# Kernel tuning notes

Measured on AMD Instinct MI355X. Metric: run time of the kernel, lower is better.

## Reference

```python
import jax, jax.numpy as jnp
import numpy as np

B, T, P, C = 32, 16, 16, 2048
EPS = 1e-5


def setup_inputs() -> dict:
    key = jax.random.key(0)
    ks = jax.random.split(key, 9)
    s = 0.02
    return {
        "X": jax.random.normal(ks[0], (B, T, P, C), dtype=jnp.float32),
        "W_att": jax.random.normal(ks[1], (C, C), dtype=jnp.float32) * s,
        "b_att": jnp.zeros((C,), dtype=jnp.float32),
        "W1": jax.random.normal(ks[2], (C, C), dtype=jnp.float32) * s,
        "b1": jnp.zeros((C,), dtype=jnp.float32),
        "gamma": jnp.ones((C,), dtype=jnp.float32),
        "beta": jnp.zeros((C,), dtype=jnp.float32),
        "W2": jax.random.normal(ks[3], (C, C), dtype=jnp.float32) * s,
        "b2": jnp.zeros((C,), dtype=jnp.float32),
    }


def reference(X, W_att, b_att, W1, b1, gamma, beta, W2, b2):
    b, t, p, c = X.shape
    Xf = X.reshape(b * t, p, c)                                   # [BT, P, C]
    # per-frame attention gate: mean over parts -> Linear -> sigmoid
    attn = jax.nn.sigmoid(jnp.einsum("nc,dc->nd", Xf.mean(axis=1), W_att) + b_att)
    Xg = Xf * attn[:, None, :]                                    # gate each part
    # gcn: Linear -> per-frame BatchNorm1d (training stats over P) -> ReLU -> Linear
    h = jnp.einsum("npc,dc->npd", Xg, W1) + b1                    # [BT, P, C]
    mu = h.mean(axis=1, keepdims=True)
    var = jnp.mean(jnp.square(h - mu), axis=1, keepdims=True)     # biased var, as torch BN
    hn = (h - mu) * jax.lax.rsqrt(var + EPS) * gamma + beta
    out = jnp.einsum("npc,dc->npd", jax.nn.relu(hn), W2) + b2
    return out.reshape(b, t, p, c)
```

## Files before the change

kernel.cpp:

```cpp
#include <hip/hip_runtime.h>
#include <hip/hip_bf16.h>

typedef __attribute__((ext_vector_type(8))) short short8;
typedef __attribute__((ext_vector_type(4))) float f32x4;

static constexpr int Cdim = 2048;
static constexpr int NFRM = 512;
static constexpr int Pdim = 16;
static constexpr int MROWS = NFRM * Pdim;
static constexpr float EPS = 1e-5f;

__device__ __forceinline__ unsigned short f2b(float x) {
  union { float f; unsigned u; } v; v.f = x;
  unsigned r = v.u + 0x7fffu + ((v.u >> 16) & 1u);
  return (unsigned short)(r >> 16);
}

__device__ __forceinline__ void gload16(const void* g, void* l) {
  __builtin_amdgcn_global_load_lds(
      (const __attribute__((address_space(1))) unsigned int*)g,
      (__attribute__((address_space(3))) unsigned int*)l, 16, 0, 0);
}


__global__ __launch_bounds__(256) void cast3_kernel(
    const float* __restrict__ s0, const float* __restrict__ s1, const float* __restrict__ s2,
    unsigned short* __restrict__ d0, unsigned short* __restrict__ d1, unsigned short* __restrict__ d2)
{
  long i = (long)blockIdx.x * 256 + threadIdx.x;
  const float* s; unsigned short* d; long off;
  if (i < 1048576)      { s = s0; d = d0; off = i; }
  else if (i < 2097152) { s = s1; d = d1; off = i - 1048576; }
  else                  { s = s2; d = d2; off = i - 2097152; }
  float4 v = reinterpret_cast<const float4*>(s)[off];
  union { unsigned short u[4]; unsigned long long q; } o;
  o.u[0] = f2b(v.x); o.u[1] = f2b(v.y); o.u[2] = f2b(v.z); o.u[3] = f2b(v.w);
  *reinterpret_cast<unsigned long long*>(d + off * 4) = o.q;
}

__global__ __launch_bounds__(256) void mean_cast_kernel(
    const float* __restrict__ X, unsigned short* __restrict__ Mb)
{
  int idx = blockIdx.x * 256 + threadIdx.x;
  int n  = idx >> 9;
  int c4 = idx & 511;
  const float4* xp = reinterpret_cast<const float4*>(X) + (long)n * (Pdim * 512) + c4;
  float4 s = {0.f, 0.f, 0.f, 0.f};
  #pragma unroll
  for (int p = 0; p < Pdim; ++p) {
    float4 v = xp[(long)p * 512];
    s.x += v.x; s.y += v.y; s.z += v.z; s.w += v.w;
  }
  const float r = 1.f / 16.f;
  union { unsigned short u[4]; unsigned long long q; } o;
  o.u[0] = f2b(s.x * r); o.u[1] = f2b(s.y * r); o.u[2] = f2b(s.z * r); o.u[3] = f2b(s.w * r);
  *reinterpret_cast<unsigned long long*>(Mb + (long)idx * 4) = o.q;
}

__global__ __launch_bounds__(256) void gate_kernel(
    const float* __restrict__ X, const float* __restrict__ PA, const float* __restrict__ PB,
    const float* __restrict__ b_att, unsigned short* __restrict__ Xg)
{
  constexpr long F = 512L * 2048;
  long idx = (long)blockIdx.x * 256 + threadIdx.x;
  int c4 = (int)(idx & 511);
  long np = idx >> 9;
  long n  = np >> 4;
  float4 x  = reinterpret_cast<const float4*>(X)[idx];
  float4 p0 = reinterpret_cast<const float4*>(PA)[n * 512 + c4];
  float4 p1 = reinterpret_cast<const float4*>(PA + F)[n * 512 + c4];
  float4 p2 = reinterpret_cast<const float4*>(PB)[n * 512 + c4];
  float4 p3 = reinterpret_cast<const float4*>(PB + F)[n * 512 + c4];
  float4 bb = reinterpret_cast<const float4*>(b_att)[c4];
  float4 a;
  a.x = 1.f / (1.f + __expf(-(p0.x + p1.x + p2.x + p3.x + bb.x)));
  a.y = 1.f / (1.f + __expf(-(p0.y + p1.y + p2.y + p3.y + bb.y)));
  a.z = 1.f / (1.f + __expf(-(p0.z + p1.z + p2.z + p3.z + bb.z)));
  a.w = 1.f / (1.f + __expf(-(p0.w + p1.w + p2.w + p3.w + bb.w)));
  union { unsigned short u[4]; unsigned long long q; } o;
  o.u[0] = f2b(x.x * a.x); o.u[1] = f2b(x.y * a.y);
  o.u[2] = f2b(x.z * a.z); o.u[3] = f2b(x.w * a.w);
  *reinterpret_cast<unsigned long long*>(Xg + idx * 4) = o.q;
}

__global__ __launch_bounds__(256) void gemm_att_sk(
    const unsigned short* __restrict__ A,
    const unsigned short* __restrict__ B,
    float* __restrict__ PA, float* __restrict__ PB)
{
  constexpr int N = 2048, K = 2048, KH = 512;
  constexpr long F = 512L * 2048;
  __shared__ unsigned short As[128 * 32];
  __shared__ unsigned short Bs[128 * 32];
  const int t = threadIdx.x;
  const int lane = t & 63;
  const int wid = t >> 6;
  const int wr = wid >> 1, wc = wid & 1;
  const int m0 = blockIdx.x * 128, n0 = blockIdx.y * 128;
  const int k0 = blockIdx.z * KH;
  float* out = (blockIdx.z < 2) ? (PA + (long)blockIdx.z * F) : (PB + (long)(blockIdx.z - 2) * F);

  f32x4 acc[4][4];
  #pragma unroll
  for (int i = 0; i < 4; i++)
    #pragma unroll
    for (int j = 0; j < 4; j++) acc[i][j] = (f32x4){0.f, 0.f, 0.f, 0.f};

  const int srow = t >> 2;
  const int scol = (t & 3) * 8;
  const long aoff0 = (long)(m0 + srow) * K + scol;
  const long aoff1 = (long)(m0 + 64 + srow) * K + scol;
  const long boff0 = (long)(n0 + srow) * K + scol;
  const long boff1 = (long)(n0 + 64 + srow) * K + scol;
  char* AsB = (char*)As;
  char* BsB = (char*)Bs;

  const int fr = lane & 15;
  const int fk = (lane >> 4) * 8;

  for (int kt = k0; kt < k0 + KH; kt += 32) {
    __syncthreads();
    gload16(A + aoff0 + kt, AsB + t * 16);
    gload16(A + aoff1 + kt, AsB + 4096 + t * 16);
    gload16(B + boff0 + kt, BsB + t * 16);
    gload16(B + boff1 + kt, BsB + 4096 + t * 16);
    __syncthreads();
    short8 af[4], bfr[4];
    #pragma unroll
    for (int m = 0; m < 4; m++)
      af[m] = *reinterpret_cast<const short8*>(&As[(wr * 64 + m * 16 + fr) * 32 + fk]);
    #pragma unroll
    for (int n = 0; n < 4; n++)
      bfr[n] = *reinterpret_cast<const short8*>(&Bs[(wc * 64 + n * 16 + fr) * 32 + fk]);
    #pragma unroll
    for (int m = 0; m < 4; m++)
      #pragma unroll
      for (int n = 0; n < 4; n++)
        acc[m][n] = __builtin_amdgcn_mfma_f32_16x16x32_bf16(af[m], bfr[n], acc[m][n], 0, 0, 0);
  }

  const int l4 = lane >> 4;
  #pragma unroll
  for (int m = 0; m < 4; m++) {
    const int r0 = m0 + wr * 64 + m * 16 + l4 * 4;
    #pragma unroll
    for (int n = 0; n < 4; n++) {
      const int cn = n0 + wc * 64 + n * 16 + fr;
      #pragma unroll
      for (int j = 0; j < 4; j++)
        out[(long)(r0 + j) * N + cn] = acc[m][n][j];
    }
  }
}

template<int EPI>
__global__ __launch_bounds__(512, 2) void gemm256(
    const unsigned short* __restrict__ A,
    const unsigned short* __restrict__ Bp,
    int Kk, int Nn, int nbx,
    const float* __restrict__ bias,
    const float* __restrict__ gamma,
    const float* __restrict__ beta,
    float* __restrict__ Cf,
    unsigned short* __restrict__ Cb)
{
  __shared__ char lds[131072];
  const int t = threadIdx.x;
  const int lane = t & 63;
  const int wid = t >> 6;
  const int wr = wid >> 2;
  const int wc = wid & 3;

  const int nw = gridDim.x;
  const int wg = (blockIdx.x & 7) * (nw >> 3) + (blockIdx.x >> 3);
  const int bx = wg % nbx;
  const int by = wg / nbx;
  const int m0 = bx << 8, n0 = by << 8;

  const int NT = Kk >> 6;
  const int NI = NT >> 1;

  const long h64 = (long)64 * Kk, h128 = (long)128 * Kk;
  const int row0 = t >> 3;
  const int col0 = ((t & 7) * 8) ^ ((row0 & 7) << 3);
  const unsigned short* gA = A  + (long)(m0 + row0) * Kk + col0;
  const unsigned short* gB = Bp + (long)(n0 + row0) * Kk + col0;

  const int fr_ = lane & 15;
  const int cb0 = ((lane >> 4) << 4) ^ ((fr_ & 7) << 4);
  const int aB = (wr << 14) + fr_ * 128;
  const int bB = 32768 + ((wc >> 1) << 14) + ((wc & 1) << 13) + fr_ * 128;

#define STG(gp_, ko_, lo_) do { \
    const unsigned short* g0_ = (gp_) + (ko_); \
    gload16(g0_, lds + (lo_) + (t << 4)); \
    gload16(g0_ + h64, lds + (lo_) + 8192 + (t << 4)); } while (0)

#define LDSA(buf_, m_, ks_) (*(const short8*)(lds + (buf_) * 65536 + aB + (m_) * 2048 + (cb0 ^ ((ks_) << 6))))
#define LDSB(buf_, n_, ks_) (*(const short8*)(lds + (buf_) * 65536 + bB + (n_) * 2048 + (cb0 ^ ((ks_) << 6))))

#define RDAF(buf_, mb_) do { \
    af[0][0] = LDSA(buf_, (mb_) + 0, 0); af[0][1] = LDSA(buf_, (mb_) + 0, 1); \
    af[1][0] = LDSA(buf_, (mb_) + 1, 0); af[1][1] = LDSA(buf_, (mb_) + 1, 1); \
    af[2][0] = LDSA(buf_, (mb_) + 2, 0); af[2][1] = LDSA(buf_, (mb_) + 2, 1); \
    af[3][0] = LDSA(buf_, (mb_) + 3, 0); af[3][1] = LDSA(buf_, (mb_) + 3, 1); } while (0)

#define RDB(buf_, nb_, dst_) do { \
    dst_[0][0] = LDSB(buf_, (nb_) + 0, 0); dst_[0][1] = LDSB(buf_, (nb_) + 0, 1); \
    dst_[1][0] = LDSB(buf_, (nb_) + 1, 0); dst_[1][1] = LDSB(buf_, (nb_) + 1, 1); } while (0)

#define QUAD(mb_, nb_, b_) do { \
    _Pragma("unroll") \
    for (int mi = 0; mi < 4; ++mi) { \
      _Pragma("unroll") \
      for (int ni = 0; ni < 2; ++ni) { \
        acc[(mb_) + mi][(nb_) + ni] = __builtin_amdgcn_mfma_f32_16x16x32_bf16(af[mi][0], b_[ni][0], acc[(mb_) + mi][(nb_) + ni], 0, 0, 0); \
        acc[(mb_) + mi][(nb_) + ni] = __builtin_amdgcn_mfma_f32_16x16x32_bf16(af[mi][1], b_[ni][1], acc[(mb_) + mi][(nb_) + ni], 0, 0, 0); \
      } } } while (0)

#define BARX() do { \
    __builtin_amdgcn_sched_barrier(0); \
    __builtin_amdgcn_s_barrier(); \
    __builtin_amdgcn_sched_barrier(0); } while (0)

#define PRIO1() __builtin_amdgcn_s_setprio(1)
#define PRIO0() __builtin_amdgcn_s_setprio(0)
#define VMC(n_) asm volatile("s_waitcnt vmcnt(" #n_ ")" ::: "memory")

  f32x4 acc[8][4];
  #pragma unroll
  for (int i = 0; i < 8; i++)
    #pragma unroll
    for (int j = 0; j < 4; j++) acc[i][j] = (f32x4){0.f, 0.f, 0.f, 0.f};

  short8 af[4][2], b23[2][2], bE0[2][2], bO0[2][2];

  STG(gA, 0, 0);
  STG(gA + h128, 0, 16384);
  STG(gB, 0, 32768);
  STG(gB + h128, 0, 49152);
  STG(gB, 64, 98304);
  STG(gB + h128, 64, 114688);
  VMC(4);
  __builtin_amdgcn_s_barrier();
  __builtin_amdgcn_sched_barrier(0);
  RDB(0, 0, bE0);

#define ITERBODY(LAST_) do { \
     \
    STG(gA, ko + 64, 65536); \
    RDAF(0, 0); \
    BARX(); PRIO1(); QUAD(0, 0, bE0); PRIO0(); \
     \
    STG(gA + h128, ko + 64, 81920); \
    RDB(0, 2, b23); \
    BARX(); PRIO1(); QUAD(0, 2, b23); PRIO0(); \
     \
    VMC(4); \
    if (!(LAST_)) STG(gB, ko + 128, 32768); \
    RDAF(0, 4); \
    BARX(); PRIO1(); QUAD(4, 0, bE0); PRIO0(); \
     \
    if (LAST_) { VMC(0); } else { VMC(2); STG(gB + h128, ko + 128, 49152); } \
    RDB(1, 0, bO0); \
    BARX(); PRIO1(); QUAD(4, 2, b23); PRIO0(); \
     \
    if (!(LAST_)) STG(gA, ko + 128, 0); \
    RDAF(1, 0); \
    BARX(); PRIO1(); QUAD(0, 0, bO0); PRIO0(); \
     \
    if (!(LAST_)) STG(gA + h128, ko + 128, 16384); \
    RDB(1, 2, b23); \
    BARX(); PRIO1(); QUAD(0, 2, b23); PRIO0(); \
     \
    if (!(LAST_)) { VMC(4); STG(gB, ko + 192, 98304); } \
    RDAF(1, 4); \
    BARX(); PRIO1(); QUAD(4, 0, bO0); PRIO0(); \
     \
    if (!(LAST_)) { VMC(2); STG(gB + h128, ko + 192, 114688); RDB(0, 0, bE0); } \
    BARX(); PRIO1(); QUAD(4, 2, b23); PRIO0(); \
  } while (0)

  long ko = 0;
  for (int i = 0; i < NI - 1; ++i, ko += 128) {
    ITERBODY(0);
  }
  ITERBODY(1);

  const int l4 = lane >> 4;
  #pragma unroll
  for (int m = 0; m < 8; ++m) {
    const int r0 = m0 + wr * 128 + m * 16 + l4 * 4;
    #pragma unroll
    for (int n = 0; n < 4; ++n) {
      const int cn = n0 + wc * 64 + n * 16 + fr_;
      if constexpr (EPI == 1) {
        float s1 = 0.f, s2 = 0.f;
        #pragma unroll
        for (int j = 0; j < 4; j++) { float v = acc[m][n][j]; s1 += v; s2 += v * v; }
        s1 += __shfl_xor(s1, 16); s2 += __shfl_xor(s2, 16);
        s1 += __shfl_xor(s1, 32); s2 += __shfl_xor(s2, 32);
        const float mean = s1 * 0.0625f;
        const float var  = s2 * 0.0625f - mean * mean;
        const float sc = rsqrtf(var + EPS) * gamma[cn];
        const float sh = beta[cn] - mean * sc;
        #pragma unroll
        for (int j = 0; j < 4; j++) {
          float v = fmaxf(acc[m][n][j] * sc + sh, 0.f);
          Cb[(long)(r0 + j) * Nn + cn] = f2b(v);
        }
      } else {
        const float bb = bias[cn];
        #pragma unroll
        for (int j = 0; j < 4; j++)
          Cf[(long)(r0 + j) * Nn + cn] = acc[m][n][j] + bb;
      }
    }
  }
#undef STG
#undef LDSA
#undef LDSB
#undef RDAF
#undef RDB
#undef QUAD
#undef BARX
#undef PRIO1
#undef PRIO0
#undef VMC
#undef ITERBODY
}

extern "C" void kernel_launch(void* const* d_in, const int* in_sizes, int n_in,
                              void* d_out, int out_size, void* d_ws, size_t ws_size,
                              hipStream_t stream) {
  const float* X     = (const float*)d_in[0];
  const float* W_att = (const float*)d_in[1];
  const float* b_att = (const float*)d_in[2];
  const float* W1    = (const float*)d_in[3];
  const float* gamma = (const float*)d_in[5];
  const float* beta  = (const float*)d_in[6];
  const float* W2    = (const float*)d_in[7];
  const float* b2    = (const float*)d_in[8];
  float* out = (float*)d_out;

  char* ws = (char*)d_ws;
  unsigned short* Wab = (unsigned short*)(ws + 0);
  unsigned short* W1b = (unsigned short*)(ws + 8388608);
  unsigned short* W2b = (unsigned short*)(ws + 16777216);
  float*          PatA= (float*)        (ws + 25165824);
  unsigned short* Xg  = (unsigned short*)(ws + 33554432);
  unsigned short* Hr  = (unsigned short*)(ws + 67108864);
  unsigned short* Mb  = (unsigned short*)(ws + 67108864);
  float*          PatB= (float*)        (ws + 67108864 + 2097152);

  hipLaunchKernelGGL(cast3_kernel, dim3(12288), dim3(256), 0, stream,
                     W_att, W1, W2, Wab, W1b, W2b);
  hipLaunchKernelGGL(mean_cast_kernel, dim3(1024), dim3(256), 0, stream, X, Mb);
  hipLaunchKernelGGL(gemm_att_sk, dim3(4, 16, 4), dim3(256), 0, stream,
                     Mb, Wab, PatA, PatB);
  hipLaunchKernelGGL(gate_kernel, dim3(16384), dim3(256), 0, stream,
                     X, PatA, PatB, b_att, Xg);
  hipLaunchKernelGGL((gemm256<1>), dim3(256), dim3(512), 0, stream,
                     Xg, W1b, Cdim, Cdim, 32, nullptr, gamma, beta, nullptr, Hr);
  hipLaunchKernelGGL((gemm256<2>), dim3(256), dim3(512), 0, stream,
                     Hr, W2b, Cdim, Cdim, 32, b2, nullptr, nullptr, out, nullptr);
}
```

Baseline: 183.9 us.

## Fuse weight cast with mean kernel, store split-K partials in bf16, regroup A staging

The weight-cast and frame-mean kernels become a single launch that branches on block index, saving one launch and its tail. The split-K attention GEMM now writes its partial sums as bf16 instead of fp32, which halves partial traffic for both the writer and the gate kernel. In the main GEMM pipeline, both halves of the A-tile loads are issued together earlier in the step. Rounding the partials to bf16 adds some error to the attention logits.

```diff
diff --git a/kernel.cpp b/kernel.cpp
--- a/kernel.cpp
+++ b/kernel.cpp
@@ -16,49 +16,54 @@
   return (unsigned short)(r >> 16);
 }
 
+__device__ __forceinline__ float b2f(unsigned short b) {
+  union { float f; unsigned u; } v; v.u = (unsigned)b << 16;
+  return v.f;
+}
+
 __device__ __forceinline__ void gload16(const void* g, void* l) {
   __builtin_amdgcn_global_load_lds(
       (const __attribute__((address_space(1))) unsigned int*)g,
       (__attribute__((address_space(3))) unsigned int*)l, 16, 0, 0);
 }
 
-
-__global__ __launch_bounds__(256) void cast3_kernel(
+__global__ __launch_bounds__(256) void prep0_kernel(
     const float* __restrict__ s0, const float* __restrict__ s1, const float* __restrict__ s2,
-    unsigned short* __restrict__ d0, unsigned short* __restrict__ d1, unsigned short* __restrict__ d2)
-{
-  long i = (long)blockIdx.x * 256 + threadIdx.x;
-  const float* s; unsigned short* d; long off;
-  if (i < 1048576)      { s = s0; d = d0; off = i; }
-  else if (i < 2097152) { s = s1; d = d1; off = i - 1048576; }
-  else                  { s = s2; d = d2; off = i - 2097152; }
-  float4 v = reinterpret_cast<const float4*>(s)[off];
-  union { unsigned short u[4]; unsigned long long q; } o;
-  o.u[0] = f2b(v.x); o.u[1] = f2b(v.y); o.u[2] = f2b(v.z); o.u[3] = f2b(v.w);
-  *reinterpret_cast<unsigned long long*>(d + off * 4) = o.q;
-}
-
-__global__ __launch_bounds__(256) void mean_cast_kernel(
+    unsigned short* __restrict__ d0, unsigned short* __restrict__ d1, unsigned short* __restrict__ d2,
     const float* __restrict__ X, unsigned short* __restrict__ Mb)
 {
-  int idx = blockIdx.x * 256 + threadIdx.x;
-  int n  = idx >> 9;
-  int c4 = idx & 511;
-  const float4* xp = reinterpret_cast<const float4*>(X) + (long)n * (Pdim * 512) + c4;
-  float4 s = {0.f, 0.f, 0.f, 0.f};
-  #pragma unroll
-  for (int p = 0; p < Pdim; ++p) {
-    float4 v = xp[(long)p * 512];
-    s.x += v.x; s.y += v.y; s.z += v.z; s.w += v.w;
-  }
-  const float r = 1.f / 16.f;
-  union { unsigned short u[4]; unsigned long long q; } o;
-  o.u[0] = f2b(s.x * r); o.u[1] = f2b(s.y * r); o.u[2] = f2b(s.z * r); o.u[3] = f2b(s.w * r);
-  *reinterpret_cast<unsigned long long*>(Mb + (long)idx * 4) = o.q;
+  const int bid = blockIdx.x;
+  if (bid < 12288) {
+    long i = (long)bid * 256 + threadIdx.x;
+    const float* s; unsigned short* d; long off;
+    if (i < 1048576)      { s = s0; d = d0; off = i; }
+    else if (i < 2097152) { s = s1; d = d1; off = i - 1048576; }
+    else                  { s = s2; d = d2; off = i - 2097152; }
+    float4 v = reinterpret_cast<const float4*>(s)[off];
+    union { unsigned short u[4]; unsigned long long q; } o;
+    o.u[0] = f2b(v.x); o.u[1] = f2b(v.y); o.u[2] = f2b(v.z); o.u[3] = f2b(v.w);
+    *reinterpret_cast<unsigned long long*>(d + off * 4) = o.q;
+  } else {
+    int idx = (bid - 12288) * 256 + threadIdx.x;
+    int n  = idx >> 9;
+    int c4 = idx & 511;
+    const float4* xp = reinterpret_cast<const float4*>(X) + (long)n * (Pdim * 512) + c4;
+    float4 s = {0.f, 0.f, 0.f, 0.f};
+    #pragma unroll
+    for (int p = 0; p < Pdim; ++p) {
+      float4 v = xp[(long)p * 512];
+      s.x += v.x; s.y += v.y; s.z += v.z; s.w += v.w;
+    }
+    const float r = 1.f / 16.f;
+    union { unsigned short u[4]; unsigned long long q; } o;
+    o.u[0] = f2b(s.x * r); o.u[1] = f2b(s.y * r); o.u[2] = f2b(s.z * r); o.u[3] = f2b(s.w * r);
+    *reinterpret_cast<unsigned long long*>(Mb + (long)idx * 4) = o.q;
+  }
 }
 
 __global__ __launch_bounds__(256) void gate_kernel(
-    const float* __restrict__ X, const float* __restrict__ PA, const float* __restrict__ PB,
+    const float* __restrict__ X, const unsigned short* __restrict__ PA,
+    const unsigned short* __restrict__ PB,
     const float* __restrict__ b_att, unsigned short* __restrict__ Xg)
 {
   constexpr long F = 512L * 2048;
@@ -67,16 +72,16 @@
   long np = idx >> 9;
   long n  = np >> 4;
   float4 x  = reinterpret_cast<const float4*>(X)[idx];
-  float4 p0 = reinterpret_cast<const float4*>(PA)[n * 512 + c4];
-  float4 p1 = reinterpret_cast<const float4*>(PA + F)[n * 512 + c4];
-  float4 p2 = reinterpret_cast<const float4*>(PB)[n * 512 + c4];
-  float4 p3 = reinterpret_cast<const float4*>(PB + F)[n * 512 + c4];
+  ushort4 q0 = reinterpret_cast<const ushort4*>(PA)[n * 512 + c4];
+  ushort4 q1 = reinterpret_cast<const ushort4*>(PA + F)[n * 512 + c4];
+  ushort4 q2 = reinterpret_cast<const ushort4*>(PB)[n * 512 + c4];
+  ushort4 q3 = reinterpret_cast<const ushort4*>(PB + F)[n * 512 + c4];
   float4 bb = reinterpret_cast<const float4*>(b_att)[c4];
   float4 a;
-  a.x = 1.f / (1.f + __expf(-(p0.x + p1.x + p2.x + p3.x + bb.x)));
-  a.y = 1.f / (1.f + __expf(-(p0.y + p1.y + p2.y + p3.y + bb.y)));
-  a.z = 1.f / (1.f + __expf(-(p0.z + p1.z + p2.z + p3.z + bb.z)));
-  a.w = 1.f / (1.f + __expf(-(p0.w + p1.w + p2.w + p3.w + bb.w)));
+  a.x = 1.f / (1.f + __expf(-(b2f(q0.x) + b2f(q1.x) + b2f(q2.x) + b2f(q3.x) + bb.x)));
+  a.y = 1.f / (1.f + __expf(-(b2f(q0.y) + b2f(q1.y) + b2f(q2.y) + b2f(q3.y) + bb.y)));
+  a.z = 1.f / (1.f + __expf(-(b2f(q0.z) + b2f(q1.z) + b2f(q2.z) + b2f(q3.z) + bb.z)));
+  a.w = 1.f / (1.f + __expf(-(b2f(q0.w) + b2f(q1.w) + b2f(q2.w) + b2f(q3.w) + bb.w)));
   union { unsigned short u[4]; unsigned long long q; } o;
   o.u[0] = f2b(x.x * a.x); o.u[1] = f2b(x.y * a.y);
   o.u[2] = f2b(x.z * a.z); o.u[3] = f2b(x.w * a.w);
@@ -86,7 +91,7 @@
 __global__ __launch_bounds__(256) void gemm_att_sk(
     const unsigned short* __restrict__ A,
     const unsigned short* __restrict__ B,
-    float* __restrict__ PA, float* __restrict__ PB)
+    unsigned short* __restrict__ PA, unsigned short* __restrict__ PB)
 {
   constexpr int N = 2048, K = 2048, KH = 512;
   constexpr long F = 512L * 2048;
@@ -98,7 +103,7 @@
   const int wr = wid >> 1, wc = wid & 1;
   const int m0 = blockIdx.x * 128, n0 = blockIdx.y * 128;
   const int k0 = blockIdx.z * KH;
-  float* out = (blockIdx.z < 2) ? (PA + (long)blockIdx.z * F) : (PB + (long)(blockIdx.z - 2) * F);
+  unsigned short* out = (blockIdx.z < 2) ? (PA + (long)blockIdx.z * F) : (PB + (long)(blockIdx.z - 2) * F);
 
   f32x4 acc[4][4];
   #pragma unroll
@@ -148,7 +153,7 @@
       const int cn = n0 + wc * 64 + n * 16 + fr;
       #pragma unroll
       for (int j = 0; j < 4; j++)
-        out[(long)(r0 + j) * N + cn] = acc[m][n][j];
+        out[(long)(r0 + j) * N + cn] = f2b(acc[m][n][j]);
     }
   }
 }
@@ -249,10 +254,10 @@
 #define ITERBODY(LAST_) do { \
      \
     STG(gA, ko + 64, 65536); \
+    STG(gA + h128, ko + 64, 81920); \
     RDAF(0, 0); \
     BARX(); PRIO1(); QUAD(0, 0, bE0); PRIO0(); \
      \
-    STG(gA + h128, ko + 64, 81920); \
     RDB(0, 2, b23); \
     BARX(); PRIO1(); QUAD(0, 2, b23); PRIO0(); \
      \
@@ -265,11 +270,10 @@
     RDB(1, 0, bO0); \
     BARX(); PRIO1(); QUAD(4, 2, b23); PRIO0(); \
      \
-    if (!(LAST_)) STG(gA, ko + 128, 0); \
+    if (!(LAST_)) { STG(gA, ko + 128, 0); STG(gA + h128, ko + 128, 16384); } \
     RDAF(1, 0); \
     BARX(); PRIO1(); QUAD(0, 0, bO0); PRIO0(); \
      \
-    if (!(LAST_)) STG(gA + h128, ko + 128, 16384); \
     RDB(1, 2, b23); \
     BARX(); PRIO1(); QUAD(0, 2, b23); PRIO0(); \
      \
@@ -347,15 +351,14 @@
   unsigned short* Wab = (unsigned short*)(ws + 0);
   unsigned short* W1b = (unsigned short*)(ws + 8388608);
   unsigned short* W2b = (unsigned short*)(ws + 16777216);
-  float*          PatA= (float*)        (ws + 25165824);
+  unsigned short* PatA= (unsigned short*)(ws + 25165824);
   unsigned short* Xg  = (unsigned short*)(ws + 33554432);
   unsigned short* Hr  = (unsigned short*)(ws + 67108864);
   unsigned short* Mb  = (unsigned short*)(ws + 67108864);
-  float*          PatB= (float*)        (ws + 67108864 + 2097152);
-
-  hipLaunchKernelGGL(cast3_kernel, dim3(12288), dim3(256), 0, stream,
-                     W_att, W1, W2, Wab, W1b, W2b);
-  hipLaunchKernelGGL(mean_cast_kernel, dim3(1024), dim3(256), 0, stream, X, Mb);
+  unsigned short* PatB= (unsigned short*)(ws + 67108864 + 2097152);
+
+  hipLaunchKernelGGL(prep0_kernel, dim3(13312), dim3(256), 0, stream,
+                     W_att, W1, W2, Wab, W1b, W2b, X, Mb);
   hipLaunchKernelGGL(gemm_att_sk, dim3(4, 16, 4), dim3(256), 0, stream,
                      Mb, Wab, PatA, PatB);
   hipLaunchKernelGGL(gate_kernel, dim3(16384), dim3(256), 0, stream,
```

Result: faster. 176.5 us, median of 3 (-4.0%).
